# Kernel optimization log

Measured on AMD Instinct MI355X. Metric: run time of the kernel, lower is better.

The kernel has to match this reference:

```python
import jax, jax.numpy as jnp
import numpy as np

N = 1024  # num boxes (labels == predictions count so diff == 0 branch)


def jaccard(box_a, box_b):
    # box_a: [A,4], box_b: [B,4], xyxy format -> IoU matrix [A,B]
    max_xy = jnp.minimum(box_a[:, None, 2:], box_b[None, :, 2:])
    min_xy = jnp.maximum(box_a[:, None, :2], box_b[None, :, :2])
    inter_wh = jnp.clip(max_xy - min_xy, 0.0)
    inter = inter_wh[..., 0] * inter_wh[..., 1]
    area_a = ((box_a[:, 2] - box_a[:, 0]) * (box_a[:, 3] - box_a[:, 1]))[:, None]
    area_b = ((box_b[:, 2] - box_b[:, 0]) * (box_b[:, 3] - box_b[:, 1]))[None, :]
    return inter / (area_a + area_b - inter)


def greedy_match(JM):
    """Replicates the original greedy loop: N steps; each step takes the LAST
    row-major-order maximal entry ('>=' update) among rows/cols not in `seen`,
    swaps label rows r<->c (tracked via perm), and marks column c as seen."""
    n = JM.shape[0]
    MASKED = jnp.float32(-1.0)  # IoU >= 0, so -1 excludes masked entries

    def body(carry, _):
        perm, seen = carry
        M = JM[perm]                                  # rows permuted with labels
        mask = seen[:, None] | seen[None, :]          # one `seen` set for rows & cols
        vals = jnp.where(mask, MASKED, M).reshape(-1)
        # last occurrence of the max (the '>=' in the Python loop keeps the latest)
        i = vals.shape[0] - 1 - jnp.argmax(vals[::-1])
        r, c = i // n, i % n
        pr, pc = perm[r], perm[c]
        perm = perm.at[r].set(pc).at[c].set(pr)
        seen = seen.at[c].set(True)
        return (perm, seen), None

    init = (jnp.arange(n), jnp.zeros(n, dtype=bool))
    (perm, _), _ = jax.lax.scan(body, init, None, length=n)
    return perm


def setup_inputs() -> dict:
    key = jax.random.key(0)
    k1, k2, k3, k4, k5 = jax.random.split(key, 5)
    # valid xyxy boxes: x2 > x1, y2 > y1
    lmin = jax.random.uniform(k1, (N, 2), dtype=jnp.float32)
    lwh = jax.random.uniform(k2, (N, 2), dtype=jnp.float32) * 0.2 + 0.01
    labels = jnp.concatenate([lmin, lmin + lwh], axis=-1)
    pmin = jax.random.uniform(k3, (N, 2), dtype=jnp.float32)
    pwh = jax.random.uniform(k4, (N, 2), dtype=jnp.float32) * 0.2 + 0.01
    predictions = jnp.concatenate([pmin, pmin + pwh], axis=-1)
    scores = jax.random.normal(k5, (N,), dtype=jnp.float32)
    return {"predictions": predictions, "labels": labels, "scores": scores}


def reference(predictions, labels, scores):
    # L == P -> diff == 0, no truncation, scores untouched.
    JM = jaccard(labels, predictions)
    perm = greedy_match(JM)
    labels_matched = labels[perm]
    # F.l1_loss default reduction: mean over all elements.
    # NOTE: the original's `loss.add(F.cross_entropy(...))` is non-in-place and
    # its result is discarded, so the CE term does NOT contribute; diff == 0 so
    # the diff*4 branch is skipped. Faithfully: loss = L1 only.
    loss = jnp.mean(jnp.abs(labels_matched - predictions))
    return loss
```

## Files before the change

kernel.cpp:

```cpp
#include <hip/hip_runtime.h>
#include <stdint.h>

#define NBOX 1024
#define BLK  512

typedef unsigned long long u64;
typedef unsigned int u32;
typedef unsigned short u16;
typedef unsigned char u8;

__device__ __forceinline__ float iou_pair(const float4 lb, float larea,
                                          const float4 pb, float parea) {
    float ix1 = fmaxf(lb.x, pb.x);
    float iy1 = fmaxf(lb.y, pb.y);
    float ix2 = fminf(lb.z, pb.z);
    float iy2 = fminf(lb.w, pb.w);
    float w = fmaxf(__fsub_rn(ix2, ix1), 0.0f);
    float h = fmaxf(__fsub_rn(iy2, iy1), 0.0f);
    float inter = __fmul_rn(w, h);
    float denom = __fsub_rn(__fadd_rn(larea, parea), inter);
    return inter / denom;
}

__device__ __forceinline__ u64 umax64(u64 a, u64 b) { return a > b ? a : b; }

__device__ __forceinline__ u64 dpp_max64(u64 v) {
    unsigned lo, hi; u64 o;
#define DPP_STEP(CTRL) \
    lo = (unsigned)__builtin_amdgcn_update_dpp(0, (int)(unsigned)(v & 0xffffffffull), CTRL, 0xf, 0xf, true); \
    hi = (unsigned)__builtin_amdgcn_update_dpp(0, (int)(unsigned)(v >> 32),           CTRL, 0xf, 0xf, true); \
    o = (((u64)hi) << 32) | lo; \
    if (o > v) v = o;
    DPP_STEP(0x111) DPP_STEP(0x112) DPP_STEP(0x114)
    DPP_STEP(0x118) DPP_STEP(0x142) DPP_STEP(0x143)
#undef DPP_STEP
    return v;
}

__device__ __forceinline__ u64 readlane64(u64 v, int l) {
    unsigned lo = (unsigned)__builtin_amdgcn_readlane((int)(unsigned)(v & 0xffffffffull), l);
    unsigned hi = (unsigned)__builtin_amdgcn_readlane((int)(unsigned)(v >> 32), l);
    return (((u64)hi) << 32) | lo;
}

__global__ void __launch_bounds__(64) init_rowlist(const float* __restrict__ labels,
                                                   const float* __restrict__ preds,
                                                   u64* __restrict__ rowlist) {
    const int b = blockIdx.x;
    const int lane = threadIdx.x;
    float4 lb = ((const float4*)labels)[b];
    float la = __fmul_rn(__fsub_rn(lb.z, lb.x), __fsub_rn(lb.w, lb.y));
    u32 vb[16];
    #pragma unroll
    for (int j = 0; j < 16; ++j) {
        int c = lane + (j << 6);
        float4 pb = ((const float4*)preds)[c];
        float pa = __fmul_rn(__fsub_rn(pb.z, pb.x), __fsub_rn(pb.w, pb.y));
        vb[j] = __float_as_uint(iou_pair(lb, la, pb, pa));
    }
    u32 used = 0;
    for (int it = 0; it < 8; ++it) {
        u64 best = 0;
        #pragma unroll
        for (int j = 0; j < 16; ++j) {
            if (!((used >> j) & 1u)) {
                u64 p = ((u64)vb[j] << 10) | (u32)(lane + (j << 6));
                best = umax64(best, p);
            }
        }
        best = dpp_max64(best);
        u64 bm = readlane64(best, 63);
        if ((bm >> 10) == 0ull) bm = 0;
        if (lane == 0) rowlist[(b << 3) + it] = bm;
        if (bm && (int)(bm & 63) == lane) used |= 1u << ((bm >> 6) & 15);
    }
}

__global__ void __launch_bounds__(64) init_collist(const float* __restrict__ labels,
                                                   const float* __restrict__ preds,
                                                   u64* __restrict__ collist) {
    const int c = blockIdx.x;
    const int lane = threadIdx.x;
    float4 pc = ((const float4*)preds)[c];
    float pa = __fmul_rn(__fsub_rn(pc.z, pc.x), __fsub_rn(pc.w, pc.y));
    u32 vb[16];
    #pragma unroll
    for (int j = 0; j < 16; ++j) {
        int L = lane + (j << 6);
        float4 lb = ((const float4*)labels)[L];
        float la = __fmul_rn(__fsub_rn(lb.z, lb.x), __fsub_rn(lb.w, lb.y));
        vb[j] = __float_as_uint(iou_pair(lb, la, pc, pa));
    }
    u32 used = 0;
    for (int it = 0; it < 8; ++it) {
        u64 best = 0;
        #pragma unroll
        for (int j = 0; j < 16; ++j) {
            if (!((used >> j) & 1u)) {
                u64 p = ((u64)vb[j] << 10) | (u32)(lane + (j << 6));
                best = umax64(best, p);
            }
        }
        best = dpp_max64(best);
        u64 bm = readlane64(best, 63);
        if ((bm >> 10) == 0ull) bm = 0;
        if (lane == 0) collist[(c << 3) + it] = bm;
        if (bm && (int)(bm & 63) == lane) used |= 1u << ((bm >> 6) & 15);
    }
}

__global__ void __launch_bounds__(BLK, 1)
rounds_kernel(const float* __restrict__ preds,
              const float* __restrict__ labels,
              const u64* __restrict__ rowlist,
              const u64* __restrict__ collist,
              float* __restrict__ out) {
    __shared__ float4 pred4s[NBOX];
    __shared__ float4 lab4s[NBOX];
    __shared__ float  parea_s[NBOX];
    __shared__ float  larea_s[NBOX];
    __shared__ u64    rkey[NBOX];
    __shared__ u64    colbest[NBOX];
    __shared__ u16    dest_s[NBOX];
    __shared__ u16    perm_s[NBOX];
    __shared__ u8     seenc[NBOX];
    __shared__ u8     lockedl[NBOX];
    __shared__ u32    seenw[32];
    __shared__ u32    lockedw[32];
    __shared__ int    ncom[2];
    __shared__ float  fpart[8];

    const int t    = (int)threadIdx.x;
    const int lane = t & 63;
    const int wid  = t >> 6;

    #pragma unroll
    for (int s = 0; s < 2; ++s) {
        int i = t + (s << 9);
        float4 p = ((const float4*)preds)[i];
        float4 L = ((const float4*)labels)[i];
        pred4s[i] = p;
        lab4s[i]  = L;
        parea_s[i] = __fmul_rn(__fsub_rn(p.z, p.x), __fsub_rn(p.w, p.y));
        larea_s[i] = __fmul_rn(__fsub_rn(L.z, L.x), __fsub_rn(L.w, L.y));
        perm_s[i] = (u16)i; dest_s[i] = 0;
        seenc[i] = 0; lockedl[i] = 0;
        rkey[i] = rowlist ? rowlist[i << 3] : 0ull;
        colbest[i] = 0ull;
    }
    if (t < 32) { seenw[t] = 0u; lockedw[t] = 0u; }
    if (t < 2) ncom[t] = 0;
    __syncthreads();

    u32 cvA[8], clA[8], cvB[8], clB[8];
    if (collist) {
        #pragma unroll
        for (int k = 0; k < 8; ++k) {
            u64 e = collist[(t << 3) + k];
            cvA[k] = (u32)(e >> 10); clA[k] = (u32)(e & 1023ull);
            e = collist[((t + 512) << 3) + k];
            cvB[k] = (u32)(e >> 10); clB[k] = (u32)(e & 1023ull);
        }
    } else {
        #pragma unroll
        for (int k = 0; k < 8; ++k) { cvA[k] = clA[k] = cvB[k] = clB[k] = 0; }
    }

    u32 myseen = 0;
    u32 mylocked = 0;
    int rptr0 = rowlist ? 0 : 8;
    int rptr1 = rowlist ? 0 : 8;
    int par = 0;
    const bool havelists = (collist != nullptr);

    auto rebuild_seen = [&]() {
        u32 ms = 0;
        #pragma unroll
        for (int m = 0; m < 4; ++m) {
            u32 w_ = seenw[(lane >> 3) + (m << 3)];
            ms |= ((w_ >> ((lane & 7) << 2)) & 0xFu) << (m << 2);
        }
        myseen = ms;
    };
    auto rebuild_locked = [&]() {
        u32 ml = 0;
        #pragma unroll
        for (int m = 0; m < 4; ++m) {
            u32 w_ = lockedw[(lane >> 3) + (m << 3)];
            ml |= ((w_ >> ((lane & 7) << 2)) & 0xFu) << (m << 2);
        }
        mylocked = ml;
    };

    auto scan_row_exact = [&](int row) -> u64 {
        float4 lbx = lab4s[row];
        float la = larea_s[row];
        u64 best = 0;
        #pragma unroll
        for (int m = 0; m < 4; ++m) {
            #pragma unroll
            for (int k = 0; k < 4; ++k) {
                int cc = 4 * lane + 256 * m + k;
                float v = iou_pair(lbx, la, pred4s[cc], parea_s[cc]);
                u64 p = ((u64)__float_as_uint(v) << 10) | (unsigned)cc;
                if ((myseen >> ((m << 2) | k)) & 1u) p = 0;
                best = umax64(best, p);
            }
        }
        best = dpp_max64(best);
        u64 bm = readlane64(best, 63);
        return (bm >> 10) ? bm : 0ull;
    };

    auto scan_col_exact = [&](int c) -> u64 {
        float4 pc = pred4s[c];
        float  pa = parea_s[c];
        u64 best = 0; u32 v1 = 0, v2 = 0;
        #pragma unroll
        for (int m = 0; m < 4; ++m) {
            #pragma unroll
            for (int k = 0; k < 4; ++k) {
                int L = 4 * lane + 256 * m + k;
                float v = iou_pair(lab4s[L], larea_s[L], pc, pa);
                u32 vbb = __float_as_uint(v);
                if ((mylocked >> ((m << 2) | k)) & 1u) vbb = 0;
                if (vbb >= v1) { v2 = v1; v1 = vbb; } else { v2 = (vbb > v2) ? vbb : v2; }
                best = umax64(best, ((u64)vbb << 10) | (unsigned)L);
            }
        }
        best = dpp_max64(best);
        u64 bm = readlane64(best, 63);
        u32 V = (u32)(bm >> 10);
        if (!V) return 0ull;
        u64 b1 = __ballot(v1 == V);
        u64 b2 = __ballot(v2 == V);
        bool tie = (__popcll(b1) >= 2) || (b2 != 0ull);
        return ((u64)V << 32) | (tie ? (1ull << 16) : 0ull) | (bm & 1023ull);
    };

    auto do_commit = [&](int c, int L) {
        seenc[c] = 1; lockedl[L] = 1; rkey[L] = 0ull;
        dest_s[L] = (u16)c; perm_s[c] = (u16)L;
        atomicOr(&seenw[c >> 5], 1u << (c & 31));
        atomicOr(&lockedw[L >> 5], 1u << (L & 31));
        atomicAdd(&ncom[par], 1);
    };

#define COLWALK(CV, CL, cidx, sbv, needx) do { \
        if (!havelists) { needx = true; } else { \
            bool lk_[8]; \
            _Pragma("unroll") \
            for (int k = 0; k < 8; ++k) lk_[k] = lockedl[CL[k]]; \
            u32 fm_ = 0; \
            _Pragma("unroll") \
            for (int k = 0; k < 8; ++k) if (CV[k] && !lk_[k]) fm_ |= 1u << k; \
            if (!fm_) { if (CV[7]) needx = true;  } \
            else { \
                u32 V_ = 0, lab_ = 0; \
                _Pragma("unroll") \
                for (int k = 7; k >= 0; --k) \
                    if ((fm_ >> k) & 1u) { V_ = CV[k]; lab_ = CL[k]; } \
                u32 eq_ = 0; \
                _Pragma("unroll") \
                for (int k = 0; k < 8; ++k) if (CV[k] == V_) eq_ |= 1u << k; \
                bool tie_ = __popc(fm_ & eq_) >= 2; \
                if (!tie_) { \
                    if (CV[7] == V_) needx = true;               \
                    else if ((u32)((sbv) & 1023ull) == lab_) do_commit((cidx), (int)lab_); \
                }  \
            } \
        } } while (0)

    if (!rowlist) {
        for (int row = wid; row < NBOX; row += 8) {
            u64 r = scan_row_exact(row);
            if (lane == 0) rkey[row] = r;
        }
        __syncthreads();
    }

    #pragma unroll
    for (int s = 0; s < 2; ++s) {
        u64 k = rkey[t + (s << 9)];
        if (k) atomicMax((unsigned long long*)&colbest[k & 1023ull],
                         ((k >> 10) << 10) | (u64)(unsigned)(t + (s << 9)));
    }
    __syncthreads();

    for (int round = 0; round < 4096; ++round) {
        par = round & 1;

        {
            u64 sb0 = colbest[t];       colbest[t] = 0ull;
            u64 sb1 = colbest[t + 512]; colbest[t + 512] = 0ull;
            bool ne0 = false, ne1 = false;
            if (sb0) COLWALK(cvA, clA, t, sb0, ne0);
            if (sb1) COLWALK(cvB, clB, t + 512, sb1, ne1);
            u64 bal = __ballot(ne0);
            if (bal) {
                rebuild_locked();
                while (bal) {
                    int l = (int)__ffsll(bal) - 1; bal &= bal - 1;
                    int c = (wid << 6) | l;
                    u64 o = scan_col_exact(c);
                    u64 sbl = readlane64(sb0, l);
                    if (lane == 0) {
                        if ((o >> 32) && !((o >> 16) & 1ull) &&
                            (u32)(o & 1023ull) == (u32)(sbl & 1023ull))
                            do_commit(c, (int)(o & 1023ull));
                    }
                }
            }
            bal = __ballot(ne1);
            if (bal) {
                rebuild_locked();
                while (bal) {
                    int l = (int)__ffsll(bal) - 1; bal &= bal - 1;
                    int c = 512 + ((wid << 6) | l);
                    u64 o = scan_col_exact(c);
                    u64 sbl = readlane64(sb1, l);
                    if (lane == 0) {
                        if ((o >> 32) && !((o >> 16) & 1ull) &&
                            (u32)(o & 1023ull) == (u32)(sbl & 1023ull))
                            do_commit(c, (int)(o & 1023ull));
                    }
                }
            }
        }
        __syncthreads();

        const int cnt = ncom[par];
        if (t == 0) ncom[par ^ 1] = 0;
        if (cnt == 0) break;
        {
            bool ns0 = false, ns1 = false;
            #pragma unroll
            for (int s = 0; s < 2; ++s) {
                int row = t + (s << 9);
                int rp = s ? rptr1 : rptr0;
                bool needscan = false;
                u64 k = rkey[row];
                if (k && seenc[k & 1023ull]) {
                    if (rp >= 8) {
                        needscan = true;
                    } else {
                        int i = rp; u64 nk = 0;
                        for (; i < 8; ++i) {
                            u64 e = rowlist[(row << 3) + i];
                            if ((e >> 10) == 0ull) break;
                            if (!seenc[e & 1023ull]) { nk = e; break; }
                        }
                        if (i < 8) { rkey[row] = nk; rp = i; }
                        else { rp = 8; needscan = true; }
                    }
                }
                if (s) { rptr1 = rp; ns1 = needscan; } else { rptr0 = rp; ns0 = needscan; }
            }
            u64 bal = __ballot(ns0);
            if (bal) {
                rebuild_seen();
                while (bal) {
                    int l = (int)__ffsll(bal) - 1; bal &= bal - 1;
                    int row = (wid << 6) | l;
                    u64 r = scan_row_exact(row);
                    if (lane == 0) rkey[row] = r;
                }
            }
            bal = __ballot(ns1);
            if (bal) {
                rebuild_seen();
                while (bal) {
                    int l = (int)__ffsll(bal) - 1; bal &= bal - 1;
                    int row = 512 + ((wid << 6) | l);
                    u64 r = scan_row_exact(row);
                    if (lane == 0) rkey[row] = r;
                }
            }
            #pragma unroll
            for (int s = 0; s < 2; ++s) {
                int row = t + (s << 9);
                u64 k2 = rkey[row];
                if (k2) atomicMax((unsigned long long*)&colbest[k2 & 1023ull],
                                  ((k2 >> 10) << 10) | (u64)(unsigned)row);
            }
        }
        __syncthreads();
    }

    #pragma unroll
    for (int s = 0; s < 2; ++s) {
        int i = t + (s << 9);
        if (!seenc[i]) {
            int l = i;
            while (lockedl[l]) l = (int)dest_s[l];
            perm_s[i] = (u16)l;
        }
    }
    __syncthreads();

    {
        float sum = 0.0f;
        #pragma unroll
        for (int s = 0; s < 2; ++s) {
            int i = t + (s << 9);
            float4 lb = lab4s[perm_s[i]];
            float4 pb = pred4s[i];
            sum += fabsf(lb.x - pb.x) + fabsf(lb.y - pb.y) +
                   fabsf(lb.z - pb.z) + fabsf(lb.w - pb.w);
        }
        for (int off = 32; off > 0; off >>= 1) sum += __shfl_xor(sum, off, 64);
        if (lane == 0) fpart[wid] = sum;
        __syncthreads();
        if (t == 0) {
            float s = 0.0f;
            for (int w = 0; w < 8; ++w) s += fpart[w];
            out[0] = s * (1.0f / 4096.0f);
        }
    }
}

extern "C" void kernel_launch(void* const* d_in, const int* in_sizes, int n_in,
                              void* d_out, int out_size, void* d_ws, size_t ws_size,
                              hipStream_t stream) {
    const float* preds  = (const float*)d_in[0];
    const float* labels = (const float*)d_in[1];
    float* out = (float*)d_out;

    const size_t list_b = (size_t)NBOX * 8 * sizeof(u64);
    if (d_ws && ws_size >= 2 * list_b) {
        u64* rl = (u64*)d_ws;
        u64* cl = rl + NBOX * 8;
        init_rowlist<<<NBOX, 64, 0, stream>>>(labels, preds, rl);
        init_collist<<<NBOX, 64, 0, stream>>>(labels, preds, cl);
        rounds_kernel<<<1, BLK, 0, stream>>>(preds, labels, rl, cl, out);
    } else {
        rounds_kernel<<<1, BLK, 0, stream>>>(preds, labels, nullptr, nullptr, out);
    }
}
```

Measured before the change: 223.5 us.

## Keep row keys and row candidate lists in registers, use bitmask seen/locked state

Moves per-row current best keys and the 8-entry row candidate lists from shared/global memory into per-thread registers. It also replaces the byte arrays for seen columns and locked labels with the existing bitmask words. This removes repeated global loads of rowlist inside the round loop and some shared-memory traffic. In exchange it raises register pressure with 32 more u32 registers per thread. The row-promotion walk also gets more complex, with a new early clear for locked rows.

```diff
diff --git a/kernel.cpp b/kernel.cpp
--- a/kernel.cpp
+++ b/kernel.cpp
@@ -119,12 +119,9 @@
     __shared__ float4 lab4s[NBOX];
     __shared__ float  parea_s[NBOX];
     __shared__ float  larea_s[NBOX];
-    __shared__ u64    rkey[NBOX];
     __shared__ u64    colbest[NBOX];
     __shared__ u16    dest_s[NBOX];
     __shared__ u16    perm_s[NBOX];
-    __shared__ u8     seenc[NBOX];
-    __shared__ u8     lockedl[NBOX];
     __shared__ u32    seenw[32];
     __shared__ u32    lockedw[32];
     __shared__ int    ncom[2];
@@ -144,34 +141,46 @@
         parea_s[i] = __fmul_rn(__fsub_rn(p.z, p.x), __fsub_rn(p.w, p.y));
         larea_s[i] = __fmul_rn(__fsub_rn(L.z, L.x), __fsub_rn(L.w, L.y));
         perm_s[i] = (u16)i; dest_s[i] = 0;
-        seenc[i] = 0; lockedl[i] = 0;
-        rkey[i] = rowlist ? rowlist[i << 3] : 0ull;
         colbest[i] = 0ull;
     }
     if (t < 32) { seenw[t] = 0u; lockedw[t] = 0u; }
     if (t < 2) ncom[t] = 0;
     __syncthreads();
 
+    const bool havelists = (collist != nullptr);
+
     u32 cvA[8], clA[8], cvB[8], clB[8];
-    if (collist) {
+    u32 rvA[8], rcA[8], rvB[8], rcB[8];
+    if (havelists) {
         #pragma unroll
         for (int k = 0; k < 8; ++k) {
             u64 e = collist[(t << 3) + k];
             cvA[k] = (u32)(e >> 10); clA[k] = (u32)(e & 1023ull);
             e = collist[((t + 512) << 3) + k];
             cvB[k] = (u32)(e >> 10); clB[k] = (u32)(e & 1023ull);
+            e = rowlist[(t << 3) + k];
+            rvA[k] = (u32)(e >> 10); rcA[k] = (u32)(e & 1023ull);
+            e = rowlist[((t + 512) << 3) + k];
+            rvB[k] = (u32)(e >> 10); rcB[k] = (u32)(e & 1023ull);
         }
     } else {
         #pragma unroll
-        for (int k = 0; k < 8; ++k) { cvA[k] = clA[k] = cvB[k] = clB[k] = 0; }
-    }
+        for (int k = 0; k < 8; ++k) {
+            cvA[k] = clA[k] = cvB[k] = clB[k] = 0;
+            rvA[k] = rcA[k] = rvB[k] = rcB[k] = 0;
+        }
+    }
+
+    u64 rk0 = havelists ? (((u64)rvA[0] << 10) | rcA[0]) : 0ull;
+    u64 rk1 = havelists ? (((u64)rvB[0] << 10) | rcB[0]) : 0ull;
+    if ((rk0 >> 10) == 0ull) rk0 = 0;
+    if ((rk1 >> 10) == 0ull) rk1 = 0;
+    int rptr0 = havelists ? 0 : 8;
+    int rptr1 = havelists ? 0 : 8;
 
     u32 myseen = 0;
     u32 mylocked = 0;
-    int rptr0 = rowlist ? 0 : 8;
-    int rptr1 = rowlist ? 0 : 8;
     int par = 0;
-    const bool havelists = (collist != nullptr);
 
     auto rebuild_seen = [&]() {
         u32 ms = 0;
@@ -239,7 +248,6 @@
     };
 
     auto do_commit = [&](int c, int L) {
-        seenc[c] = 1; lockedl[L] = 1; rkey[L] = 0ull;
         dest_s[L] = (u16)c; perm_s[c] = (u16)L;
         atomicOr(&seenw[c >> 5], 1u << (c & 31));
         atomicOr(&lockedw[L >> 5], 1u << (L & 31));
@@ -250,7 +258,8 @@
         if (!havelists) { needx = true; } else { \
             bool lk_[8]; \
             _Pragma("unroll") \
-            for (int k = 0; k < 8; ++k) lk_[k] = lockedl[CL[k]]; \
+            for (int k = 0; k < 8; ++k) \
+                lk_[k] = (lockedw[CL[k] >> 5] >> (CL[k] & 31)) & 1u; \
             u32 fm_ = 0; \
             _Pragma("unroll") \
             for (int k = 0; k < 8; ++k) if (CV[k] && !lk_[k]) fm_ |= 1u << k; \
@@ -271,20 +280,46 @@
             } \
         } } while (0)
 
-    if (!rowlist) {
+#define PROMOTE(RK, RP, RV, RC, rowv, needs) do { \
+        if (RK) { \
+            if ((lockedw[(rowv) >> 5] >> ((rowv) & 31)) & 1u) { RK = 0; } \
+            else { \
+                u32 c_ = (u32)(RK & 1023ull); \
+                if ((seenw[c_ >> 5] >> (c_ & 31)) & 1u) { \
+                    if (RP >= 8) { needs = true; } \
+                    else { \
+                        u32 vm_ = 0, zm_ = 0; \
+                        _Pragma("unroll") \
+                        for (int k = 0; k < 8; ++k) { \
+                            bool sn_ = (seenw[RC[k] >> 5] >> (RC[k] & 31)) & 1u; \
+                            if (RV[k] == 0) zm_ |= 1u << k; \
+                            else if (!sn_) vm_ |= 1u << k; \
+                        } \
+                        vm_ &= ~((1u << RP) - 1); \
+                        u32 lim_ = zm_ ? ((1u << (__ffs(zm_) - 1)) - 1) : 0xFFu; \
+                        u32 cand_ = vm_ & lim_; \
+                        if (cand_) { int k_ = __ffs(cand_) - 1; \
+                            RK = ((u64)RV[k_] << 10) | RC[k_]; RP = k_; } \
+                        else if (zm_) { RK = 0; } \
+                        else { RP = 8; needs = true; } \
+                    } \
+                } \
+            } \
+        } } while (0)
+
+    if (!havelists) {
         for (int row = wid; row < NBOX; row += 8) {
             u64 r = scan_row_exact(row);
-            if (lane == 0) rkey[row] = r;
+            if (lane == (row & 63) && (row < 512 ? t == row : t == row - 512)) {}
+            if ((row & 511) == t) { if (row < 512) rk0 = r; else rk1 = r; }
         }
         __syncthreads();
     }
 
-    #pragma unroll
-    for (int s = 0; s < 2; ++s) {
-        u64 k = rkey[t + (s << 9)];
-        if (k) atomicMax((unsigned long long*)&colbest[k & 1023ull],
-                         ((k >> 10) << 10) | (u64)(unsigned)(t + (s << 9)));
-    }
+    if (rk0) atomicMax((unsigned long long*)&colbest[rk0 & 1023ull],
+                       ((rk0 >> 10) << 10) | (u64)(unsigned)t);
+    if (rk1) atomicMax((unsigned long long*)&colbest[rk1 & 1023ull],
+                       ((rk1 >> 10) << 10) | (u64)(unsigned)(t + 512));
     __syncthreads();
 
     for (int round = 0; round < 4096; ++round) {
@@ -334,28 +369,8 @@
         if (cnt == 0) break;
         {
             bool ns0 = false, ns1 = false;
-            #pragma unroll
-            for (int s = 0; s < 2; ++s) {
-                int row = t + (s << 9);
-                int rp = s ? rptr1 : rptr0;
-                bool needscan = false;
-                u64 k = rkey[row];
-                if (k && seenc[k & 1023ull]) {
-                    if (rp >= 8) {
-                        needscan = true;
-                    } else {
-                        int i = rp; u64 nk = 0;
-                        for (; i < 8; ++i) {
-                            u64 e = rowlist[(row << 3) + i];
-                            if ((e >> 10) == 0ull) break;
-                            if (!seenc[e & 1023ull]) { nk = e; break; }
-                        }
-                        if (i < 8) { rkey[row] = nk; rp = i; }
-                        else { rp = 8; needscan = true; }
-                    }
-                }
-                if (s) { rptr1 = rp; ns1 = needscan; } else { rptr0 = rp; ns0 = needscan; }
-            }
+            PROMOTE(rk0, rptr0, rvA, rcA, t, ns0);
+            PROMOTE(rk1, rptr1, rvB, rcB, t + 512, ns1);
             u64 bal = __ballot(ns0);
             if (bal) {
                 rebuild_seen();
@@ -363,7 +378,7 @@
                     int l = (int)__ffsll(bal) - 1; bal &= bal - 1;
                     int row = (wid << 6) | l;
                     u64 r = scan_row_exact(row);
-                    if (lane == 0) rkey[row] = r;
+                    if (lane == l) rk0 = r;
                 }
             }
             bal = __ballot(ns1);
@@ -373,16 +388,13 @@
                     int l = (int)__ffsll(bal) - 1; bal &= bal - 1;
                     int row = 512 + ((wid << 6) | l);
                     u64 r = scan_row_exact(row);
-                    if (lane == 0) rkey[row] = r;
+                    if (lane == l) rk1 = r;
                 }
             }
-            #pragma unroll
-            for (int s = 0; s < 2; ++s) {
-                int row = t + (s << 9);
-                u64 k2 = rkey[row];
-                if (k2) atomicMax((unsigned long long*)&colbest[k2 & 1023ull],
-                                  ((k2 >> 10) << 10) | (u64)(unsigned)row);
-            }
+            if (rk0) atomicMax((unsigned long long*)&colbest[rk0 & 1023ull],
+                               ((rk0 >> 10) << 10) | (u64)(unsigned)t);
+            if (rk1) atomicMax((unsigned long long*)&colbest[rk1 & 1023ull],
+                               ((rk1 >> 10) << 10) | (u64)(unsigned)(t + 512));
         }
         __syncthreads();
     }
@@ -390,9 +402,9 @@
     #pragma unroll
     for (int s = 0; s < 2; ++s) {
         int i = t + (s << 9);
-        if (!seenc[i]) {
+        if (!((seenw[i >> 5] >> (i & 31)) & 1u)) {
             int l = i;
-            while (lockedl[l]) l = (int)dest_s[l];
+            while ((lockedw[l >> 5] >> (l & 31)) & 1u) l = (int)dest_s[l];
             perm_s[i] = (u16)l;
         }
     }
```

Result: no change. 223.5 us (-0.0%).
